# Kernel optimization log

Hardware: AMD Instinct MI355X
Metric: run time of the kernel (lower is better)

The kernel has to match this reference:

```python
import jax, jax.numpy as jnp
import numpy as np
import math

B, T, D = 2, 512, 1024
H, HD = 16, 64
F = 4096
L = 2
R = 32
LOOP_DIM = 64
TEMB = 256
MAXIT = 8
TOPK = 0.55
EPS = 1e-6


def _ste(x, q):
    # straight-through estimator: forward = q, backward = identity
    return x + jax.lax.stop_gradient(q - x)


def bitlinear(x, w, topk_ratio=None):
    # BitNet b1.58 fake-quant: ternary weights (per-tensor absmean scale),
    # int8 per-token absmax activations; optional topk activation sparsity.
    s = jnp.mean(jnp.abs(w)) + 1e-8
    wq = _ste(w, jnp.clip(jnp.round(w / s), -1.0, 1.0) * s)
    if topk_ratio is not None:
        k = max(1, int(math.ceil(topk_ratio * x.shape[-1])))
        ax = jnp.abs(x)
        thr = jax.lax.top_k(ax, k)[0][..., -1:]
        x = jnp.where(ax >= thr, x, 0.0)
    a = jnp.maximum(jnp.max(jnp.abs(x), axis=-1, keepdims=True), 1e-8)
    xq = _ste(x, jnp.clip(jnp.round(x * (127.0 / a)), -128.0, 127.0) * (a / 127.0))
    return xq @ wq.T


def rmsnorm(x, w):
    return x * jax.lax.rsqrt(jnp.mean(x * x, axis=-1, keepdims=True) + EPS) * w


def _rope(x):
    # x: (B,H,T,HD)
    half = HD // 2
    inv = 1.0 / (10000.0 ** (jnp.arange(half, dtype=jnp.float32) / half))
    ang = jnp.arange(x.shape[2], dtype=jnp.float32)[:, None] * inv[None, :]
    cos, sin = jnp.cos(ang), jnp.sin(ang)
    x1, x2 = x[..., :half], x[..., half:]
    return jnp.concatenate([x1 * cos - x2 * sin, x1 * sin + x2 * cos], axis=-1)


def bitblock(h, n1, wq, wk, wv, wo, n2, wg, wu, wd):
    # pre-norm attention + SwiGLU FFN, all projections BitLinear
    b, t, _ = h.shape
    a_in = rmsnorm(h, n1)
    heads = lambda p: p.reshape(b, t, H, HD).transpose(0, 2, 1, 3)
    q = _rope(heads(bitlinear(a_in, wq)))
    k = _rope(heads(bitlinear(a_in, wk)))
    v = heads(bitlinear(a_in, wv))
    scores = jnp.einsum('bhqd,bhkd->bhqk', q, k) / math.sqrt(HD)
    mask = jnp.tril(jnp.ones((t, t), dtype=bool))
    attn = jax.nn.softmax(jnp.where(mask, scores, -1e9), axis=-1)
    o = jnp.einsum('bhqk,bhkd->bhqd', attn, v).transpose(0, 2, 1, 3).reshape(b, t, D)
    h = h + bitlinear(o, wo)
    f_in = rmsnorm(h, n2)
    h = h + bitlinear(jax.nn.silu(bitlinear(f_in, wg)) * bitlinear(f_in, wu), wd)
    return h


def loop_delta(i, t_emb, lp_w, lp2_w, lp2_b):
    # loop_index_inject: sinusoidal loop signal gated by t_emb, padded to D
    half = LOOP_DIM // 2
    frac = i / max(MAXIT - 1, 1)
    freqs = jnp.exp(-math.log(10000.0) * jnp.arange(half, dtype=jnp.float32) / half)
    ang = frac * freqs
    sig = jnp.concatenate([jnp.sin(ang), jnp.cos(ang)])  # (LOOP_DIM,)
    comb = sig[None, :] * (t_emb @ lp_w.T) + (t_emb @ lp2_w.T + lp2_b)  # (B,LOOP_DIM)
    return jnp.pad(comb, ((0, 0), (0, D - LOOP_DIM)))[:, None, :]  # (B,1,D)


def setup_inputs() -> dict:
    key = jax.random.key(0)
    ks = jax.random.split(key, 24)
    g = lambda k, shape, sc=0.02: sc * jax.random.normal(k, shape, dtype=jnp.float32)
    return {
        'x': jax.random.normal(ks[0], (B, T, D), dtype=jnp.float32),
        'e': jax.random.normal(ks[1], (B, T, D), dtype=jnp.float32),
        't_emb': jax.random.normal(ks[2], (B, TEMB), dtype=jnp.float32),
        'blk_norm1': jnp.ones((L, D), jnp.float32),
        'blk_wq': g(ks[3], (L, D, D)),
        'blk_wk': g(ks[4], (L, D, D)),
        'blk_wv': g(ks[5], (L, D, D)),
        'blk_wo': g(ks[6], (L, D, D)),
        'blk_norm2': jnp.ones((L, D), jnp.float32),
        'blk_wg': g(ks[7], (L, F, D)),
        'blk_wu': g(ks[8], (L, F, D)),
        'blk_wd': g(ks[9], (L, D, F)),
        'A_raw': 0.1 * jax.random.normal(ks[10], (D,), dtype=jnp.float32),
        'B_w': g(ks[11], (D, D)),
        'lora_down': g(ks[12], (R, D)),
        'lora_up': g(ks[13], (D, R)),
        'iter_gate': jnp.full((MAXIT,), 0.1, jnp.float32),
        'act_w': g(ks[14], (1, D)),
        'alpha': jnp.full((MAXIT,), 1.0 / L, jnp.float32),
        'loop_proj_w': g(ks[15], (LOOP_DIM, TEMB)),
        'loop_proj2_w': g(ks[16], (LOOP_DIM, TEMB)),
        'loop_proj2_b': jnp.zeros((LOOP_DIM,), jnp.float32),
        'loop_norm_w': jnp.ones((D,), jnp.float32),
        'n_loops': 8,
    }


def reference(x, e, t_emb, blk_norm1, blk_wq, blk_wk, blk_wv, blk_wo,
              blk_norm2, blk_wg, blk_wu, blk_wd, A_raw, B_w,
              lora_down, lora_up, iter_gate, act_w, alpha,
              loop_proj_w, loop_proj2_w, loop_proj2_b, loop_norm_w, n_loops):
    A_eff = 0.99 * jnp.tanh(A_raw)          # diagonal LTI, |A|<0.99
    Be = bitlinear(e, B_w)                  # loop-invariant anchor B(e)
    h = x
    h_out = x
    ws = []
    for i in range(int(n_loops)):
        h_in = rmsnorm(h + loop_delta(i, t_emb, loop_proj_w, loop_proj2_w, loop_proj2_b), loop_norm_w)
        bo = h_in
        for l in range(L):
            bo = bitblock(bo, blk_norm1[l], blk_wq[l], blk_wk[l], blk_wv[l], blk_wo[l],
                          blk_norm2[l], blk_wg[l], blk_wu[l], blk_wd[l])
        bo = alpha[i] * bo
        h = A_eff * h + Be + bo             # LTI injection
        h = h + iter_gate[i] * bitlinear(bitlinear(h, lora_down), lora_up, topk_ratio=TOPK)
        w = jax.nn.sigmoid(bitlinear(h, act_w))  # (B,T,1) soft ACT weight
        h_out = h_out + w * (h - h_out)     # incremental residual blend
        ws.append(w)
    ponder = jnp.mean(jnp.stack(ws))
    return h_out, ponder
```

## Files before the change

### kernel.cpp

```cpp
#include <hip/hip_runtime.h>
#include <stdint.h>

#define DEV static __device__ __forceinline__

typedef float f32x4 __attribute__((ext_vector_type(4)));
typedef int   i32x4 __attribute__((ext_vector_type(4)));
typedef unsigned short u16x8 __attribute__((ext_vector_type(8)));

DEV float bf2f(unsigned short u){ return __uint_as_float(((unsigned int)u)<<16); }
DEV unsigned short f2bfr(float f){
  unsigned int u = __float_as_uint(f);
  return (unsigned short)((u + 0x7FFF + ((u>>16)&1)) >> 16);
}
DEV signed char f2i8(float f){ return (signed char)(int)f; }

DEV float wredsum(float v){
#pragma unroll
  for (int o=32;o;o>>=1) v += __shfl_xor(v,o);
  return v;
}
DEV float wredmax(float v){
#pragma unroll
  for (int o=32;o;o>>=1) v = fmaxf(v,__shfl_xor(v,o));
  return v;
}
DEV float bredsum(float v, float* red){
  v = wredsum(v);
  if ((threadIdx.x&63)==0) red[threadIdx.x>>6] = v;
  __syncthreads();
  float r = red[0]+red[1]+red[2]+red[3];
  __syncthreads();
  return r;
}
DEV float bredmax(float v, float* red){
  v = wredmax(v);
  if ((threadIdx.x&63)==0) red[threadIdx.x>>6] = v;
  __syncthreads();
  float r = fmaxf(fmaxf(red[0],red[1]),fmaxf(red[2],red[3]));
  __syncthreads();
  return r;
}

__global__ void fill_k(float* p, int n, float v){
  int i = blockIdx.x*256 + threadIdx.x;
  if (i < n) p[i] = v;
}

__global__ __launch_bounds__(256) void setup_misc_k(const float* __restrict__ x,
                                                    float* __restrict__ h, float* __restrict__ ho,
                                                    const float* __restrict__ temb,
                                                    const float* __restrict__ lpw,
                                                    const float* __restrict__ lp2w,
                                                    const float* __restrict__ lp2b,
                                                    float* __restrict__ delta,
                                                    float* __restrict__ tab){
  __shared__ float red[4];
  int bid = blockIdx.x, t = threadIdx.x;
  if (bid < 1024){
    int i = bid*256 + t;
    float4 v = *(const float4*)(x + (size_t)i*4);
    *(float4*)(h  + (size_t)i*4) = v;
    *(float4*)(ho + (size_t)i*4) = v;
    if (i==0) ho[1048576] = 0.f;
  } else if (bid < 1152){
    int blk = bid - 1024;
    int b = blk >> 6, j = blk & 63;
    float te = temb[b*256 + t];
    float p1 = bredsum(te * lpw[j*256 + t], red);
    float p2 = bredsum(te * lp2w[j*256 + t], red);
    if (t < 8){
      int i = t;
      float frac = (float)i / 7.f;
      int jj = j & 31;
      float fr = expf(-logf(10000.f) * (float)jj * (1.f/32.f));
      float ang = frac * fr;
      float sig = (j < 32) ? sinf(ang) : cosf(ang);
      delta[i*128 + b*64 + j] = sig*p1 + p2 + lp2b[j];
    }
  } else {
    int i = (bid-1152)*256 + t;
    int tpos = i >> 5, d = i & 31;
    float inv = powf(10000.f, -(float)d * (1.f/32.f));
    float sv, cv; sincosf((float)tpos * inv, &sv, &cv);
    tab[i*2]   = cv;
    tab[i*2+1] = sv;
  }
}

struct WSetup {
  const float* src[18];
  signed char* dst[18];
  int mode[18];
};
DEV long n4of(int mat){ return mat<9 ? 262144 : (mat<15 ? 1048576 : (mat<17 ? 8192 : 256)); }

__global__ __launch_bounds__(256) void absmean_all_k(WSetup wsu, float* __restrict__ part){
  __shared__ float red[4];
  int mat = blockIdx.x >> 8;
  int seg = blockIdx.x & 255;
  long n4 = n4of(mat);
  long cnt = n4 >> 8;
  const float4* p = (const float4*)wsu.src[mat] + (long)seg*cnt;
  float s0=0.f, s1=0.f, s2=0.f, s3=0.f;
  long j = threadIdx.x;
  for (; j + 768 < cnt; j += 1024){
    float4 a = p[j], b = p[j+256], c = p[j+512], d = p[j+768];
    s0 += fabsf(a.x)+fabsf(a.y)+fabsf(a.z)+fabsf(a.w);
    s1 += fabsf(b.x)+fabsf(b.y)+fabsf(b.z)+fabsf(b.w);
    s2 += fabsf(c.x)+fabsf(c.y)+fabsf(c.z)+fabsf(c.w);
    s3 += fabsf(d.x)+fabsf(d.y)+fabsf(d.z)+fabsf(d.w);
  }
  for (; j < cnt; j += 256){
    float4 a = p[j];
    s0 += fabsf(a.x)+fabsf(a.y)+fabsf(a.z)+fabsf(a.w);
  }
  float s = bredsum(s0+s1+s2+s3, red);
  if (threadIdx.x==0) part[(long)mat*256 + seg] = s;
}

__global__ __launch_bounds__(256) void finalize_scales_k(const float* __restrict__ part,
                                                         float* __restrict__ scales){
  __shared__ float red[4];
  const long numel[18] = {1048576, 1048576,1048576, 1048576,1048576, 1048576,1048576,
                          1048576,1048576, 4194304,4194304, 4194304,4194304, 4194304,4194304,
                          32768, 32768, 1024};
  for (int m=0;m<18;m++){
    float v = part[(long)m*256 + threadIdx.x];
    v = bredsum(v, red);
    if (threadIdx.x==0) scales[m] = v/(float)numel[m] + 1e-8f;
  }
  if (threadIdx.x==0){
    for (int l=0;l<2;l++){
      scales[18+l*3+0] = scales[1+l];
      scales[18+l*3+1] = scales[3+l];
      scales[18+l*3+2] = scales[5+l];
      scales[24+l*2+0] = scales[9+l];
      scales[24+l*2+1] = scales[11+l];
    }
  }
}

__global__ __launch_bounds__(256) void quantw_all_k(WSetup wsu, const float* __restrict__ scales){
  int bid = blockIdx.x;
  int mat = 0, c = 0;
  for (;;){
    int nb = mat<9 ? 256 : (mat<15 ? 1024 : (mat<17 ? 8 : 1));
    if (bid < c + nb) break;
    c += nb; mat++;
  }
  long seg = bid - c;
  long n4 = n4of(mat);
  float s = scales[mat];
  int md = wsu.mode[mat];
  const float4* src = (const float4*)wsu.src[mat];
  char4* dst = (char4*)wsu.dst[mat];
  long base = seg*1024;
#pragma unroll
  for (int k=0;k<4;k++){
    long i = base + k*256 + threadIdx.x;
    if (i < n4){
      float4 v = src[i];
      char4 q;
      q.x = f2i8(fminf(fmaxf(rintf(v.x/s), -1.f), 1.f));
      q.y = f2i8(fminf(fmaxf(rintf(v.y/s), -1.f), 1.f));
      q.z = f2i8(fminf(fmaxf(rintf(v.z/s), -1.f), 1.f));
      q.w = f2i8(fminf(fmaxf(rintf(v.w/s), -1.f), 1.f));
      if (md == 0) dst[i] = q;
      else {
        long r = i >> 8, cc = i & 255;
        dst[(((r<<1) | (md-1))<<8) | cc] = q;
      }
    }
  }
}

__global__ __launch_bounds__(256) void rowquant1k_k(const float* __restrict__ x,
                                                    signed char* __restrict__ xq,
                                                    float* __restrict__ rs){
  __shared__ float red[4];
  int m = blockIdx.x, t = threadIdx.x;
  float v[4];
  float4 f = *(const float4*)(x + (size_t)m*1024 + t*4);
  v[0]=f.x; v[1]=f.y; v[2]=f.z; v[3]=f.w;
  float am = fmaxf(fmaxf(fabsf(v[0]),fabsf(v[1])),fmaxf(fabsf(v[2]),fabsf(v[3])));
  am = bredmax(am, red);
  float a = fmaxf(am, 1e-8f), inv = 127.f/a;
  char4 q;
  q.x = f2i8(fminf(fmaxf(rintf(v[0]*inv),-128.f),127.f));
  q.y = f2i8(fminf(fmaxf(rintf(v[1]*inv),-128.f),127.f));
  q.z = f2i8(fminf(fmaxf(rintf(v[2]*inv),-128.f),127.f));
  q.w = f2i8(fminf(fmaxf(rintf(v[3]*inv),-128.f),127.f));
  *(char4*)(xq + (size_t)m*1024 + t*4) = q;
  if (t==0) rs[m] = a/127.f;
}

__global__ __launch_bounds__(256) void rowquant4k_k(const float* __restrict__ x,
                                                    signed char* __restrict__ xq,
                                                    float* __restrict__ rs){
  __shared__ float red[4];
  int m = blockIdx.x, t = threadIdx.x;
  const float* p = x + (size_t)m*4096 + t*16;
  float v[16];
#pragma unroll
  for (int j=0;j<16;j+=4){
    float4 f = *(const float4*)(p + j);
    v[j]=f.x; v[j+1]=f.y; v[j+2]=f.z; v[j+3]=f.w;
  }
  float am = 0.f;
#pragma unroll
  for (int j=0;j<16;j++) am = fmaxf(am, fabsf(v[j]));
  am = bredmax(am, red);
  float a = fmaxf(am, 1e-8f), inv = 127.f/a;
#pragma unroll
  for (int j=0;j<16;j+=4){
    char4 q;
    q.x = f2i8(fminf(fmaxf(rintf(v[j+0]*inv),-128.f),127.f));
    q.y = f2i8(fminf(fmaxf(rintf(v[j+1]*inv),-128.f),127.f));
    q.z = f2i8(fminf(fmaxf(rintf(v[j+2]*inv),-128.f),127.f));
    q.w = f2i8(fminf(fmaxf(rintf(v[j+3]*inv),-128.f),127.f));
    *(char4*)(xq + (size_t)m*4096 + t*16 + j) = q;
  }
  if (t==0) rs[m] = a/127.f;
}

__global__ __launch_bounds__(256) void loopnorm_quant_k(const float* __restrict__ h,
                                                        const float* __restrict__ delta,
                                                        const float* __restrict__ lnw,
                                                        const float* __restrict__ n1,
                                                        float* __restrict__ hin,
                                                        signed char* __restrict__ xq,
                                                        float* __restrict__ rs){
  __shared__ float red[4];
  int m = blockIdx.x, t = threadIdx.x;
  int b = m >> 9;
  float v[4];
  float4 f = *(const float4*)(h + (size_t)m*1024 + t*4);
  v[0]=f.x; v[1]=f.y; v[2]=f.z; v[3]=f.w;
  if (t < 16){
#pragma unroll
    for (int j=0;j<4;j++) v[j] += delta[b*64 + t*4 + j];
  }
  float ss = v[0]*v[0]+v[1]*v[1]+v[2]*v[2]+v[3]*v[3];
  ss = bredsum(ss, red);
  float r1 = rsqrtf(ss*(1.f/1024.f) + 1e-6f);
  float w4[4];
#pragma unroll
  for (int j=0;j<4;j++) w4[j] = v[j]*r1*lnw[t*4+j];
  float4 of; of.x=w4[0]; of.y=w4[1]; of.z=w4[2]; of.w=w4[3];
  *(float4*)(hin + (size_t)m*1024 + t*4) = of;
  float s2 = w4[0]*w4[0]+w4[1]*w4[1]+w4[2]*w4[2]+w4[3]*w4[3];
  s2 = bredsum(s2, red);
  float r2 = rsqrtf(s2*(1.f/1024.f) + 1e-6f);
  float y[4];
#pragma unroll
  for (int j=0;j<4;j++) y[j] = w4[j]*r2*n1[t*4+j];
  float am = fmaxf(fmaxf(fabsf(y[0]),fabsf(y[1])),fmaxf(fabsf(y[2]),fabsf(y[3])));
  am = bredmax(am, red);
  float a = fmaxf(am, 1e-8f), inv = 127.f/a;
  char4 q;
  q.x = f2i8(fminf(fmaxf(rintf(y[0]*inv),-128.f),127.f));
  q.y = f2i8(fminf(fmaxf(rintf(y[1]*inv),-128.f),127.f));
  q.z = f2i8(fminf(fmaxf(rintf(y[2]*inv),-128.f),127.f));
  q.w = f2i8(fminf(fmaxf(rintf(y[3]*inv),-128.f),127.f));
  *(char4*)(xq + (size_t)m*1024 + t*4) = q;
  if (t==0) rs[m] = a/127.f;
}

DEV f32x4 accfence(f32x4 c){ asm volatile("s_nop 7\n\ts_nop 7" : "+v"(c)); return c; }
DEV i32x4 accfencei(i32x4 c){ asm volatile("s_nop 7\n\ts_nop 7" : "+v"(c)); return c; }

template<bool SPLITK, bool GUSILU>
__global__ __launch_bounds__(256)
void gemm_i8(const signed char* __restrict__ A, const signed char* __restrict__ W,
             const float* __restrict__ rowsc, const float* __restrict__ wscv,
             const float* __restrict__ res, float* __restrict__ C, int N, int Kf, int Kc)
{
  __shared__ __align__(16) signed char As[2][8192];
  __shared__ __align__(16) signed char Bs[2][8192];
  const int tid = threadIdx.x;
  const int lane = tid & 63, wvid = tid >> 6;
  const int wr = wvid >> 1, wc = wvid & 1;
  const int bm = blockIdx.y, bn = blockIdx.x;

  const int r0 = (wvid<<4) + (lane>>2);
  const int sw = (((lane&3) ^ ((r0>>1)&3)) << 4);
  const long kstart = SPLITK ? (long)blockIdx.z * Kc : 0;
  const signed char* gA = A + (size_t)(bm*128 + r0)*Kf + kstart + sw;
  const signed char* gB = W + (size_t)(bn*128 + r0)*Kf + kstart + sw;
  const size_t row64 = (size_t)64*Kf;

#define STAGE(buf, koff) do { \
    __builtin_amdgcn_global_load_lds(gA + (koff),         &As[buf][(wvid<<10)],      16, 0, 0); \
    __builtin_amdgcn_global_load_lds(gA + (koff) + row64, &As[buf][(wvid<<10)+4096], 16, 0, 0); \
    __builtin_amdgcn_global_load_lds(gB + (koff),         &Bs[buf][(wvid<<10)],      16, 0, 0); \
    __builtin_amdgcn_global_load_lds(gB + (koff) + row64, &Bs[buf][(wvid<<10)+4096], 16, 0, 0); \
  } while(0)

  i32x4 acc[4][4] = {};
  const int rA = (wr<<6) + (lane&15);
  const int rB = (wc<<6) + (lane&15);
  const int psA = (((lane>>4) ^ (((lane&15)>>1)&3)) << 4);

  STAGE(0, 0);
  const int NT = Kc >> 6;
  int cur = 0;
  for (int kt = 0; kt < NT; ++kt){
    const int knext = (kt+1 < NT) ? ((kt+1)<<6) : 0;
    STAGE(cur^1, knext);
    asm volatile("s_waitcnt vmcnt(4)" ::: "memory");
    __builtin_amdgcn_s_barrier();
    asm volatile("" ::: "memory");
    i32x4 a[4], b[4];
    const signed char* Ab = As[cur];
    const signed char* Bb = Bs[cur];
#pragma unroll
    for (int mi=0;mi<4;mi++) a[mi] = *(const i32x4*)(Ab + (rA + mi*16)*64 + psA);
#pragma unroll
    for (int ni=0;ni<4;ni++) b[ni] = *(const i32x4*)(Bb + (rB + ni*16)*64 + psA);
#pragma unroll
    for (int mi=0;mi<4;mi++)
#pragma unroll
      for (int ni=0;ni<4;ni++)
        asm("v_mfma_i32_16x16x64_i8 %0, %1, %2, %0" : "+v"(acc[mi][ni]) : "v"(a[mi]), "v"(b[ni]));
    asm volatile("s_waitcnt lgkmcnt(0)" ::: "memory");
    __builtin_amdgcn_s_barrier();
    cur ^= 1;
  }
#undef STAGE

#pragma unroll
  for (int mi=0;mi<4;mi++)
#pragma unroll
    for (int ni=0;ni<4;ni++)
      acc[mi][ni] = accfencei(acc[mi][ni]);

  const int rif = (lane>>4)<<2;
  const int cif = lane&15;
  const int gcol0 = bn*128 + (wc<<6);

  if constexpr (SPLITK){
    float* P = C + (size_t)blockIdx.z * ((size_t)N << 10);
#pragma unroll
    for (int mi=0;mi<4;mi++)
#pragma unroll
      for (int r=0;r<4;r++){
        const int grow = bm*128 + (wr<<6) + mi*16 + rif + r;
#pragma unroll
        for (int ni=0;ni<4;ni++)
          P[(size_t)grow*N + gcol0 + ni*16 + cif] = (float)acc[mi][ni][r];
      }
    return;
  }

  if constexpr (GUSILU){
    const float sg = wscv[0], su = wscv[1];
#pragma unroll
    for (int mi=0;mi<4;mi++){
#pragma unroll
      for (int r=0;r<4;r++){
        const int grow = bm*128 + (wr<<6) + mi*16 + rif + r;
        const float rsc = rowsc[grow];
#pragma unroll
        for (int ni=0;ni<4;ni++){
          const int gcol = gcol0 + ni*16 + cif;
          float val = (float)acc[mi][ni][r] * rsc * ((gcol & 1) ? su : sg);
          float other = __shfl_xor(val, 1);
          if (!(lane & 1)){
            float g = val, u = other;
            float outv = g/(1.f+expf(-g))*u;
            C[(size_t)grow*4096 + (gcol>>1)] = outv;
          }
        }
      }
    }
    return;
  }

#pragma unroll
  for (int mi=0;mi<4;mi++){
#pragma unroll
    for (int r=0;r<4;r++){
      const int grow = bm*128 + (wr<<6) + mi*16 + rif + r;
      const float rsc = rowsc[grow];
#pragma unroll
      for (int ni=0;ni<4;ni++){
        const int gcol = gcol0 + ni*16 + cif;
        float vvv = (float)acc[mi][ni][r] * rsc * wscv[0];
        const size_t off = (size_t)grow*N + gcol;
        if (res) vvv += res[off];
        C[off] = vvv;
      }
    }
  }
}

__global__ __launch_bounds__(256) void reduce4_k(const float* __restrict__ P,
                                                 const float* __restrict__ rowsc,
                                                 const float* __restrict__ wsc,
                                                 const float* __restrict__ res,
                                                 float* __restrict__ C){
  int m = blockIdx.x, t = threadIdx.x;
  float s0 = rowsc[m] * wsc[0];
  size_t off = (size_t)m*1024 + t*4;
  float4 a = *(const float4*)(P + off);
  float4 b = *(const float4*)(P + 1048576 + off);
  float4 c = *(const float4*)(P + 2097152 + off);
  float4 d = *(const float4*)(P + 3145728 + off);
  float4 o;
  o.x = (a.x+b.x+c.x+d.x)*s0;
  o.y = (a.y+b.y+c.y+d.y)*s0;
  o.z = (a.z+b.z+c.z+d.z)*s0;
  o.w = (a.w+b.w+c.w+d.w)*s0;
  if (res){
    float4 r = *(const float4*)(res + off);
    o.x += r.x; o.y += r.y; o.z += r.z; o.w += r.w;
  }
  *(float4*)(C + off) = o;
}

__global__ __launch_bounds__(256) void redq_norm_k(const float* __restrict__ P,
                                                   const float* rowsc,
                                                   const float* __restrict__ wsc,
                                                   const float* __restrict__ res,
                                                   const float* __restrict__ gamma,
                                                   float* __restrict__ Cout,
                                                   signed char* __restrict__ xq,
                                                   float* rs){
  __shared__ float red[4];
  int m = blockIdx.x, t = threadIdx.x;
  float s0 = rowsc[m] * wsc[0];
  size_t off = (size_t)m*1024 + t*4;
  float4 a = *(const float4*)(P + off);
  float4 b = *(const float4*)(P + 1048576 + off);
  float4 c = *(const float4*)(P + 2097152 + off);
  float4 d = *(const float4*)(P + 3145728 + off);
  float4 r4 = *(const float4*)(res + off);
  float v[4];
  v[0] = r4.x + (a.x+b.x+c.x+d.x)*s0;
  v[1] = r4.y + (a.y+b.y+c.y+d.y)*s0;
  v[2] = r4.z + (a.z+b.z+c.z+d.z)*s0;
  v[3] = r4.w + (a.w+b.w+c.w+d.w)*s0;
  float4 of; of.x=v[0]; of.y=v[1]; of.z=v[2]; of.w=v[3];
  *(float4*)(Cout + off) = of;
  float ss = v[0]*v[0]+v[1]*v[1]+v[2]*v[2]+v[3]*v[3];
  ss = bredsum(ss, red);
  float r1 = rsqrtf(ss*(1.f/1024.f) + 1e-6f);
  float y[4];
#pragma unroll
  for (int j=0;j<4;j++) y[j] = v[j]*r1*gamma[t*4+j];
  float am = fmaxf(fmaxf(fabsf(y[0]),fabsf(y[1])),fmaxf(fabsf(y[2]),fabsf(y[3])));
  am = bredmax(am, red);
  float aq = fmaxf(am, 1e-8f), inv = 127.f/aq;
  char4 q;
  q.x = f2i8(fminf(fmaxf(rintf(y[0]*inv),-128.f),127.f));
  q.y = f2i8(fminf(fmaxf(rintf(y[1]*inv),-128.f),127.f));
  q.z = f2i8(fminf(fmaxf(rintf(y[2]*inv),-128.f),127.f));
  q.w = f2i8(fminf(fmaxf(rintf(y[3]*inv),-128.f),127.f));
  *(char4*)(xq + (size_t)m*1024 + t*4) = q;
  if (t==0) rs[m] = aq/127.f;
}

__global__ __launch_bounds__(256) void redfin_k(const float* __restrict__ P,
                                                const float* __restrict__ rowsc,
                                                const float* __restrict__ wsc,
                                                const float* __restrict__ res,
                                                float* __restrict__ h,
                                                const float* __restrict__ Be,
                                                const float* __restrict__ Araw,
                                                const float* __restrict__ alpha, int it,
                                                const signed char* __restrict__ ldq,
                                                const float* __restrict__ sld,
                                                const signed char* __restrict__ luq,
                                                const float* __restrict__ slu,
                                                const signed char* __restrict__ actq,
                                                const float* __restrict__ sact,
                                                const float* __restrict__ ig,
                                                float* __restrict__ hout,
                                                float* __restrict__ ponder,
                                                const float* __restrict__ dnext,
                                                const float* __restrict__ lnw,
                                                const float* __restrict__ n1,
                                                float* __restrict__ hin,
                                                signed char* __restrict__ xqn,
                                                float* __restrict__ rsn,
                                                int doNext){
  __shared__ float red[4];
  __shared__ float xrow[1024];
  __shared__ float part[256];
  __shared__ float xs[32];
  __shared__ float sh_thr, sh_gs;
  int m = blockIdx.x, t = threadIdx.x;
  float al = alpha[it];
  float s0 = rowsc[m] * wsc[0];
  size_t off = (size_t)m*1024 + t*4;
  float4 a = *(const float4*)(P + off);
  float4 b = *(const float4*)(P + 1048576 + off);
  float4 c = *(const float4*)(P + 2097152 + off);
  float4 d = *(const float4*)(P + 3145728 + off);
  float4 r4 = *(const float4*)(res + off);
  float4 hh = *(const float4*)(h + off);
  float4 be = *(const float4*)(Be + off);
  float4 ar = *(const float4*)(Araw + t*4);
  float v[4];
  v[0] = 0.99f*tanhf(ar.x)*hh.x + be.x + al*(r4.x + (a.x+b.x+c.x+d.x)*s0);
  v[1] = 0.99f*tanhf(ar.y)*hh.y + be.y + al*(r4.y + (a.y+b.y+c.y+d.y)*s0);
  v[2] = 0.99f*tanhf(ar.z)*hh.z + be.z + al*(r4.z + (a.z+b.z+c.z+d.z)*s0);
  v[3] = 0.99f*tanhf(ar.w)*hh.w + be.w + al*(r4.w + (a.w+b.w+c.w+d.w)*s0);
  float am = fmaxf(fmaxf(fabsf(v[0]),fabsf(v[1])),fmaxf(fabsf(v[2]),fabsf(v[3])));
  am = bredmax(am, red);
  float aq = fmaxf(am, 1e-8f), inv = 127.f/aq;
#pragma unroll
  for (int j=0;j<4;j++) xrow[t*4+j] = fminf(fmaxf(rintf(v[j]*inv),-128.f),127.f);
  float rsv = aq/127.f;
  __syncthreads();
  {
    int r = t & 31, seg = t >> 5;
    const signed char* wrow = ldq + (size_t)r*1024 + seg*128;
    const float* xr = xrow + seg*128;
    float acc = 0.f;
    for (int k=0;k<128;k+=4){
      char4 w4 = *(const char4*)(wrow + k);
      acc += xr[k]*(float)w4.x + xr[k+1]*(float)w4.y + xr[k+2]*(float)w4.z + xr[k+3]*(float)w4.w;
    }
    part[t] = acc;
  }
  __syncthreads();
  if (t < 32){
    float s = 0.f;
    for (int sg=0; sg<8; sg++) s += part[sg*32 + t];
    xs[t] = s * rsv * (*sld);
  }
  __syncthreads();
  float val = 0.f, av = 0.f, amax = 0.f;
  if (t < 32){
    val = xs[t]; av = fabsf(val);
    int rank = 0;
    for (int j=0;j<32;j++){
      float aj = fabsf(xs[j]);
      amax = fmaxf(amax, aj);
      if (aj > av || (aj == av && j < t)) rank++;
    }
    if (rank == 17) sh_thr = av;
  }
  __syncthreads();
  if (t < 32){
    float a2 = fmaxf(amax, 1e-8f);
    float q = 0.f;
    if (av >= sh_thr) q = fminf(fmaxf(rintf(val*(127.f/a2)), -128.f), 127.f);
    xs[t] = q;
    if (t == 0) sh_gs = ig[it] * (*slu) * (a2/127.f);
  }
  __syncthreads();
  float gs = sh_gs;
  float hn[4];
  int n0 = t*4;
#pragma unroll
  for (int ni=0;ni<4;ni++){
    const signed char* lr = luq + (size_t)(n0+ni)*32;
    float dd = 0.f;
    for (int k=0;k<32;k+=4){
      char4 w4 = *(const char4*)(lr + k);
      dd += xs[k]*(float)w4.x + xs[k+1]*(float)w4.y + xs[k+2]*(float)w4.z + xs[k+3]*(float)w4.w;
    }
    hn[ni] = v[ni] + gs*dd;
  }
  float am2 = fmaxf(fmaxf(fabsf(hn[0]),fabsf(hn[1])),fmaxf(fabsf(hn[2]),fabsf(hn[3])));
  am2 = bredmax(am2, red);
  float a2 = fmaxf(am2, 1e-8f), inv2 = 127.f/a2;
  float zp = 0.f;
#pragma unroll
  for (int ni=0;ni<4;ni++){
    float q = fminf(fmaxf(rintf(hn[ni]*inv2),-128.f),127.f);
    zp += q * (float)actq[n0+ni];
  }
  zp = bredsum(zp, red);
  float z = zp * (a2/127.f) * (*sact);
  float wv = 1.f/(1.f+expf(-z));
#pragma unroll
  for (int ni=0;ni<4;ni++){
    size_t o2 = (size_t)m*1024 + n0+ni;
    float ho = hout[o2];
    hout[o2] = ho + wv*(hn[ni]-ho);
    h[o2] = hn[ni];
  }
  if (t==0) atomicAdd(ponder, wv * (1.f/8192.f));

  if (doNext){
    int b2 = m >> 9;
    float v2[4] = {hn[0], hn[1], hn[2], hn[3]};
    if (t < 16){
#pragma unroll
      for (int j=0;j<4;j++) v2[j] += dnext[b2*64 + t*4 + j];
    }
    float ss2 = v2[0]*v2[0]+v2[1]*v2[1]+v2[2]*v2[2]+v2[3]*v2[3];
    ss2 = bredsum(ss2, red);
    float r1 = rsqrtf(ss2*(1.f/1024.f) + 1e-6f);
    float w4[4];
#pragma unroll
    for (int j=0;j<4;j++) w4[j] = v2[j]*r1*lnw[t*4+j];
    float4 of; of.x=w4[0]; of.y=w4[1]; of.z=w4[2]; of.w=w4[3];
    *(float4*)(hin + off) = of;
    float s2 = w4[0]*w4[0]+w4[1]*w4[1]+w4[2]*w4[2]+w4[3]*w4[3];
    s2 = bredsum(s2, red);
    float r2 = rsqrtf(s2*(1.f/1024.f) + 1e-6f);
    float y[4];
#pragma unroll
    for (int j=0;j<4;j++) y[j] = w4[j]*r2*n1[t*4+j];
    float am3 = fmaxf(fmaxf(fabsf(y[0]),fabsf(y[1])),fmaxf(fabsf(y[2]),fabsf(y[3])));
    am3 = bredmax(am3, red);
    float aq3 = fmaxf(am3, 1e-8f), inv3 = 127.f/aq3;
    char4 q;
    q.x = f2i8(fminf(fmaxf(rintf(y[0]*inv3),-128.f),127.f));
    q.y = f2i8(fminf(fmaxf(rintf(y[1]*inv3),-128.f),127.f));
    q.z = f2i8(fminf(fmaxf(rintf(y[2]*inv3),-128.f),127.f));
    q.w = f2i8(fminf(fmaxf(rintf(y[3]*inv3),-128.f),127.f));
    *(char4*)(xqn + off) = q;
    if (t==0) rsn[m] = aq3/127.f;
  }
}

__global__ __launch_bounds__(256) void rope_reduce_k(const float* P,
                                                     const float* __restrict__ rs,
                                                     const float* __restrict__ wscv,
                                                     const float* __restrict__ tab,
                                                     unsigned short* __restrict__ C){
  int m = blockIdx.x, t = threadIdx.x;
  const float rsc = rs[m];
  const int tpos = m & 511;
  const size_t base = (size_t)m*3072;
  const float* P1 = P + 3145728;
  int p0 = t*4;
  int hh = p0 >> 5, d = p0 & 31;
  int c1 = hh*64 + d;
  float wsc = wscv[c1>>10] * rsc * ((c1 < 1024) ? 0.125f : 1.f);
  float4 xa0 = *(const float4*)(P  + base + c1);
  float4 xa1 = *(const float4*)(P1 + base + c1);
  float4 xb0 = *(const float4*)(P  + base + c1 + 32);
  float4 xb1 = *(const float4*)(P1 + base + c1 + 32);
  float4 cs01 = *(const float4*)(tab + ((size_t)tpos*32 + d)*2);
  float4 cs23 = *(const float4*)(tab + ((size_t)tpos*32 + d)*2 + 4);
  int cv = 2048 + t*4;
  float4 va = *(const float4*)(P  + base + cv);
  float4 vb = *(const float4*)(P1 + base + cv);
  float wv2 = wscv[2] * rsc;

  float x1[4] = {(xa0.x+xa1.x)*wsc, (xa0.y+xa1.y)*wsc, (xa0.z+xa1.z)*wsc, (xa0.w+xa1.w)*wsc};
  float x2[4] = {(xb0.x+xb1.x)*wsc, (xb0.y+xb1.y)*wsc, (xb0.z+xb1.z)*wsc, (xb0.w+xb1.w)*wsc};
  float cc[4] = {cs01.x, cs01.z, cs23.x, cs23.z};
  float ss[4] = {cs01.y, cs01.w, cs23.y, cs23.w};
  ushort4 o1, o2, ov;
  o1.x = f2bfr(x1[0]*cc[0] - x2[0]*ss[0]);  o2.x = f2bfr(x1[0]*ss[0] + x2[0]*cc[0]);
  o1.y = f2bfr(x1[1]*cc[1] - x2[1]*ss[1]);  o2.y = f2bfr(x1[1]*ss[1] + x2[1]*cc[1]);
  o1.z = f2bfr(x1[2]*cc[2] - x2[2]*ss[2]);  o2.z = f2bfr(x1[2]*ss[2] + x2[2]*cc[2]);
  o1.w = f2bfr(x1[3]*cc[3] - x2[3]*ss[3]);  o2.w = f2bfr(x1[3]*ss[3] + x2[3]*cc[3]);
  ov.x = f2bfr((va.x+vb.x)*wv2); ov.y = f2bfr((va.y+vb.y)*wv2);
  ov.z = f2bfr((va.z+vb.z)*wv2); ov.w = f2bfr((va.w+vb.w)*wv2);
  *(ushort4*)(C + base + c1)      = o1;
  *(ushort4*)(C + base + c1 + 32) = o2;
  *(ushort4*)(C + base + cv)      = ov;
}

DEV int swz64(int r, int c){ return r*64 + (c ^ ((r&7)<<3)); }

__global__ __launch_bounds__(256) void attn_bf16_k(const unsigned short* __restrict__ qkv,
                                                   float* __restrict__ o){
  __shared__ __align__(16) unsigned short Qs[4096];
  __shared__ __align__(16) unsigned short Ks[4096];
  __shared__ __align__(16) unsigned short Vt[4096];
  __shared__ __align__(16) unsigned short Ps[4][1024];
  const int tid = threadIdx.x;
  const int lane = tid & 63, wv = tid >> 6;
  const int qt = blockIdx.x & 7, bh = blockIdx.x >> 3;
  const int b = bh >> 4, h = bh & 15;
  const int tokb = b*512;
  const int l15 = lane & 15, lh = lane >> 4;

  {
    int r = tid >> 2, c0 = (tid & 3) << 4;
    const unsigned short* s = qkv + (size_t)(tokb + qt*64 + r)*3072 + h*64 + c0;
    u16x8 f0 = *(const u16x8*)s, f1 = *(const u16x8*)(s+8);
    *(u16x8*)(Qs + swz64(r, c0))   = f0;
    *(u16x8*)(Qs + swz64(r, c0+8)) = f1;
  }

  float m_run[4] = {-1e30f,-1e30f,-1e30f,-1e30f};
  float l_run[4] = {0.f,0.f,0.f,0.f};
  f32x4 accO[4] = {};

  for (int kt = 0; kt <= qt; ++kt){
    __syncthreads();
    {
      int r = tid >> 2, c0 = (tid & 3) << 4;
      const unsigned short* s = qkv + (size_t)(tokb + kt*64 + r)*3072 + 1024 + h*64 + c0;
      u16x8 f0 = *(const u16x8*)s, f1 = *(const u16x8*)(s+8);
      *(u16x8*)(Ks + swz64(r, c0))   = f0;
      *(u16x8*)(Ks + swz64(r, c0+8)) = f1;
    }
    {
      int r0 = (tid >> 3) << 1, cv = (tid & 7) << 3;
      const unsigned short* s0 = qkv + (size_t)(tokb + kt*64 + r0)*3072 + 2048 + h*64 + cv;
      u16x8 a = *(const u16x8*)s0;
      u16x8 b2 = *(const u16x8*)(s0 + 3072);
#pragma unroll
      for (int j=0;j<8;j++){
        int d = cv + j;
        unsigned int pk = (unsigned int)a[j] | ((unsigned int)b2[j]<<16);
        *(unsigned int*)(Vt + swz64(d, r0)) = pk;
      }
    }
    __syncthreads();

    f32x4 s4[4] = {};
#pragma unroll
    for (int kc=0; kc<2; ++kc){
      i32x4 aq = *(const i32x4*)(Qs + swz64(wv*16 + l15, kc*32 + lh*8));
#pragma unroll
      for (int nt=0; nt<4; ++nt){
        i32x4 bk = *(const i32x4*)(Ks + swz64(nt*16 + l15, kc*32 + lh*8));
        asm("v_mfma_f32_16x16x32_bf16 %0, %1, %2, %0" : "+v"(s4[nt]) : "v"(aq), "v"(bk));
      }
    }
#pragma unroll
    for (int nt=0; nt<4; ++nt) s4[nt] = accfence(s4[nt]);

    const bool diag = (kt == qt);
    float sf[4];
#pragma unroll
    for (int r=0;r<4;r++){
      int rl = lh*4 + r;
      float mx = -1e30f;
#pragma unroll
      for (int nt=0; nt<4; ++nt){
        float v = s4[nt][r];
        if (diag && (nt*16 + l15) > (wv*16 + rl)) v = -1e30f;
        s4[nt][r] = v;
        mx = fmaxf(mx, v);
      }
      mx = fmaxf(mx, __shfl_xor(mx,1));
      mx = fmaxf(mx, __shfl_xor(mx,2));
      mx = fmaxf(mx, __shfl_xor(mx,4));
      mx = fmaxf(mx, __shfl_xor(mx,8));
      float mn = fmaxf(m_run[r], mx);
      sf[r] = __expf(m_run[r] - mn);
      m_run[r] = mn;
      float ps = 0.f;
#pragma unroll
      for (int nt=0; nt<4; ++nt){
        float p = __expf(s4[nt][r] - mn);
        ps += p;
        Ps[wv][swz64(rl, nt*16 + l15)] = f2bfr(p);
      }
      ps += __shfl_xor(ps,1); ps += __shfl_xor(ps,2);
      ps += __shfl_xor(ps,4); ps += __shfl_xor(ps,8);
      l_run[r] = l_run[r]*sf[r] + ps;
    }
#pragma unroll
    for (int dt=0; dt<4; ++dt){
#pragma unroll
      for (int r=0;r<4;r++) accO[dt][r] *= sf[r];
      accO[dt] = accfence(accO[dt]);
    }
#pragma unroll
    for (int kc=0; kc<2; ++kc){
      i32x4 pa = *(const i32x4*)(Ps[wv] + swz64(l15, kc*32 + lh*8));
#pragma unroll
      for (int dt=0; dt<4; ++dt){
        i32x4 vb3 = *(const i32x4*)(Vt + swz64(dt*16 + l15, kc*32 + lh*8));
        asm("v_mfma_f32_16x16x32_bf16 %0, %1, %2, %0" : "+v"(accO[dt]) : "v"(pa), "v"(vb3));
      }
    }
  }
#pragma unroll
  for (int dt=0; dt<4; ++dt) accO[dt] = accfence(accO[dt]);
#pragma unroll
  for (int r=0;r<4;r++){
    float invl = 1.f / l_run[r];
    int row = qt*64 + wv*16 + lh*4 + r;
    float* op = o + (size_t)(tokb + row)*1024 + h*64 + l15;
#pragma unroll
    for (int dt=0; dt<4; ++dt)
      op[dt*16] = accO[dt][r] * invl;
  }
}

extern "C" void kernel_launch(void* const* d_in, const int* in_sizes, int n_in,
                              void* d_out, int out_size, void* d_ws, size_t ws_size,
                              hipStream_t stream)
{
  (void)in_sizes; (void)n_in;
  const float* x     = (const float*)d_in[0];
  const float* e     = (const float*)d_in[1];
  const float* temb  = (const float*)d_in[2];
  const float* bn1   = (const float*)d_in[3];
  const float* bwq   = (const float*)d_in[4];
  const float* bwk   = (const float*)d_in[5];
  const float* bwv   = (const float*)d_in[6];
  const float* bwo   = (const float*)d_in[7];
  const float* bn2   = (const float*)d_in[8];
  const float* bwg   = (const float*)d_in[9];
  const float* bwu   = (const float*)d_in[10];
  const float* bwd   = (const float*)d_in[11];
  const float* Araw  = (const float*)d_in[12];
  const float* Bw    = (const float*)d_in[13];
  const float* ldw   = (const float*)d_in[14];
  const float* luw   = (const float*)d_in[15];
  const float* ig    = (const float*)d_in[16];
  const float* actw  = (const float*)d_in[17];
  const float* alph  = (const float*)d_in[18];
  const float* lpw   = (const float*)d_in[19];
  const float* lp2w  = (const float*)d_in[20];
  const float* lp2b  = (const float*)d_in[21];
  const float* lnw   = (const float*)d_in[22];

  char* ws = (char*)d_ws;
  float* out = (float*)d_out;
  const size_t WS_NEEDED = 94600704ull;
  if (ws_size < WS_NEEDED){
    fill_k<<<(out_size+255)/256,256,0,stream>>>(out, out_size, 1.0e9f);
    return;
  }

  signed char* qw_qkv = (signed char*)(ws + 0);
  signed char* qw_wo  = (signed char*)(ws + 6291456);
  signed char* qw_gu  = (signed char*)(ws + 8388608);
  signed char* qw_wd  = (signed char*)(ws + 25165824);
  signed char* qw_bw  = (signed char*)(ws + 33554432);
  signed char* qw_ld  = (signed char*)(ws + 34603008);
  signed char* qw_lu  = (signed char*)(ws + 34635776);
  signed char* qw_act = (signed char*)(ws + 34668544);
  float* scales = (float*)(ws + 34669568);
  float* part   = (float*)(ws + 34670080);
  float* delta  = (float*)(ws + 34688512);
  float* hbuf   = (float*)(ws + 34692608);
  float* Bebuf  = (float*)(ws + 38886912);
  float* bufX   = (float*)(ws + 43081216);
  float* bufY   = (float*)(ws + 47275520);
  float* gub    = (float*)(ws + 51469824);
  unsigned short* qkv_bf = (unsigned short*)(ws + 76635648);
  float* obuf   = (float*)(ws + 85024256);
  signed char* xq1k = (signed char*)(ws + 89218560);
  float* rs1k   = (float*)(ws + 90267136);
  signed char* xqm  = (signed char*)(ws + 90271232);
  float* rsm    = (float*)(ws + 94465536);
  float* ropetab= (float*)(ws + 94469632);

  WSetup wsu;
  wsu.src[0]=Bw;
  wsu.src[1]=bwq; wsu.src[2]=bwq+1048576;
  wsu.src[3]=bwk; wsu.src[4]=bwk+1048576;
  wsu.src[5]=bwv; wsu.src[6]=bwv+1048576;
  wsu.src[7]=bwo; wsu.src[8]=bwo+1048576;
  wsu.src[9]=bwg; wsu.src[10]=bwg+4194304;
  wsu.src[11]=bwu; wsu.src[12]=bwu+4194304;
  wsu.src[13]=bwd; wsu.src[14]=bwd+4194304;
  wsu.src[15]=ldw; wsu.src[16]=luw; wsu.src[17]=actw;
  wsu.dst[0]=qw_bw;
  wsu.dst[1]=qw_qkv;             wsu.dst[2]=qw_qkv+3145728;
  wsu.dst[3]=qw_qkv+1048576;     wsu.dst[4]=qw_qkv+3145728+1048576;
  wsu.dst[5]=qw_qkv+2097152;     wsu.dst[6]=qw_qkv+3145728+2097152;
  wsu.dst[7]=qw_wo;              wsu.dst[8]=qw_wo+1048576;
  wsu.dst[9]=qw_gu;              wsu.dst[10]=qw_gu+8388608;
  wsu.dst[11]=qw_gu;             wsu.dst[12]=qw_gu+8388608;
  wsu.dst[13]=qw_wd;             wsu.dst[14]=qw_wd+4194304;
  wsu.dst[15]=qw_ld; wsu.dst[16]=qw_lu; wsu.dst[17]=qw_act;
  for (int i=0;i<18;i++) wsu.mode[i]=0;
  wsu.mode[9]=1;  wsu.mode[10]=1;
  wsu.mode[11]=2; wsu.mode[12]=2;

  absmean_all_k<<<4608,256,0,stream>>>(wsu, part);
  finalize_scales_k<<<1,256,0,stream>>>(part, scales);
  quantw_all_k<<<8465,256,0,stream>>>(wsu, scales);

  setup_misc_k<<<1216,256,0,stream>>>(x, hbuf, out, temb, lpw, lp2w, lp2b, delta, ropetab);

  rowquant1k_k<<<1024,256,0,stream>>>(e, xq1k, rs1k);
  { dim3 g(8,8,4); gemm_i8<true,false><<<g,256,0,stream>>>(xq1k, qw_bw, nullptr, nullptr, nullptr, gub, 1024, 1024, 256); }
  reduce4_k<<<1024,256,0,stream>>>(gub, rs1k, scales+0, nullptr, Bebuf);

  for (int it=0; it<8; ++it){
    if (it==0)
      loopnorm_quant_k<<<1024,256,0,stream>>>(hbuf, delta, lnw, bn1, bufX, xq1k, rs1k);
    for (int l=0;l<2;l++){
      { dim3 g(24,8,2); gemm_i8<true,false><<<g,256,0,stream>>>(xq1k, qw_qkv + (size_t)l*3145728, nullptr, nullptr, nullptr, gub, 3072, 1024, 512); }
      rope_reduce_k<<<1024,256,0,stream>>>(gub, rs1k, scales+18+l*3, ropetab, qkv_bf);
      attn_bf16_k<<<256,256,0,stream>>>(qkv_bf, obuf);
      rowquant1k_k<<<1024,256,0,stream>>>(obuf, xq1k, rs1k);
      { dim3 g(8,8,4); gemm_i8<true,false><<<g,256,0,stream>>>(xq1k, qw_wo + (size_t)l*1048576, nullptr, nullptr, nullptr, gub, 1024, 1024, 256); }
      redq_norm_k<<<1024,256,0,stream>>>(gub, rs1k, scales+7+l, bufX, bn2 + (size_t)l*1024, bufY, xq1k, rs1k);
      { dim3 g(64,8); gemm_i8<false,true><<<g,256,0,stream>>>(xq1k, qw_gu + (size_t)l*8388608, rs1k, scales+24+l*2, nullptr, gub, 8192, 1024, 1024); }
      rowquant4k_k<<<1024,256,0,stream>>>(gub, xqm, rsm);
      { dim3 g(8,8,4); gemm_i8<true,false><<<g,256,0,stream>>>(xqm, qw_wd + (size_t)l*4194304, nullptr, nullptr, nullptr, gub, 1024, 4096, 1024); }
      if (l==0){
        redq_norm_k<<<1024,256,0,stream>>>(gub, rsm, scales+13, bufY, bn1 + 1024, bufX, xq1k, rs1k);
      } else {
        redfin_k<<<1024,256,0,stream>>>(gub, rsm, scales+14, bufY, hbuf, Bebuf, Araw, alph, it,
                                        qw_ld, scales+15, qw_lu, scales+16, qw_act, scales+17,
                                        ig, out, out + 1048576,
                                        delta + (it+1 < 8 ? (it+1)*128 : 0), lnw, bn1, bufX, xq1k, rs1k,
                                        (it < 7) ? 1 : 0);
      }
    }
  }
}
```

Measured before the change: 2.121 ms.

## Fuse RoPE and scaling into a dedicated QKV int8 GEMM without split-K

Replaces the split-K QKV GEMM and the separate rope_reduce kernel with one GEMM that runs the full K=1024 per block. Its epilogue applies the row and weight scales and RoPE, then writes bf16 directly. This removes the fp32 partial-sum buffer round-trip and one launch per layer, at the cost of halving the grid (192 blocks) and using a longer K loop per block. It also unrolls the weight absmean reduction to issue twice as many loads per iteration on large matrices.

```diff
diff --git a/kernel.cpp b/kernel.cpp
--- a/kernel.cpp
+++ b/kernel.cpp
@@ -102,17 +102,35 @@
   long cnt = n4 >> 8;
   const float4* p = (const float4*)wsu.src[mat] + (long)seg*cnt;
   float s0=0.f, s1=0.f, s2=0.f, s3=0.f;
-  long j = threadIdx.x;
-  for (; j + 768 < cnt; j += 1024){
-    float4 a = p[j], b = p[j+256], c = p[j+512], d = p[j+768];
-    s0 += fabsf(a.x)+fabsf(a.y)+fabsf(a.z)+fabsf(a.w);
-    s1 += fabsf(b.x)+fabsf(b.y)+fabsf(b.z)+fabsf(b.w);
-    s2 += fabsf(c.x)+fabsf(c.y)+fabsf(c.z)+fabsf(c.w);
-    s3 += fabsf(d.x)+fabsf(d.y)+fabsf(d.z)+fabsf(d.w);
-  }
-  for (; j < cnt; j += 256){
-    float4 a = p[j];
-    s0 += fabsf(a.x)+fabsf(a.y)+fabsf(a.z)+fabsf(a.w);
+  if (cnt >= 2048){
+    long half = cnt >> 1;
+    const float4* q = p + half;
+    long j = threadIdx.x;
+    for (; j + 768 < half; j += 1024){
+      float4 a = p[j], b = p[j+256], c = p[j+512], d = p[j+768];
+      float4 e = q[j], f = q[j+256], g = q[j+512], h2 = q[j+768];
+      s0 += fabsf(a.x)+fabsf(a.y)+fabsf(a.z)+fabsf(a.w) + fabsf(e.x)+fabsf(e.y)+fabsf(e.z)+fabsf(e.w);
+      s1 += fabsf(b.x)+fabsf(b.y)+fabsf(b.z)+fabsf(b.w) + fabsf(f.x)+fabsf(f.y)+fabsf(f.z)+fabsf(f.w);
+      s2 += fabsf(c.x)+fabsf(c.y)+fabsf(c.z)+fabsf(c.w) + fabsf(g.x)+fabsf(g.y)+fabsf(g.z)+fabsf(g.w);
+      s3 += fabsf(d.x)+fabsf(d.y)+fabsf(d.z)+fabsf(d.w) + fabsf(h2.x)+fabsf(h2.y)+fabsf(h2.z)+fabsf(h2.w);
+    }
+    for (; j < half; j += 256){
+      float4 a = p[j], e = q[j];
+      s0 += fabsf(a.x)+fabsf(a.y)+fabsf(a.z)+fabsf(a.w) + fabsf(e.x)+fabsf(e.y)+fabsf(e.z)+fabsf(e.w);
+    }
+  } else {
+    long j = threadIdx.x;
+    for (; j + 768 < cnt; j += 1024){
+      float4 a = p[j], b = p[j+256], c = p[j+512], d = p[j+768];
+      s0 += fabsf(a.x)+fabsf(a.y)+fabsf(a.z)+fabsf(a.w);
+      s1 += fabsf(b.x)+fabsf(b.y)+fabsf(b.z)+fabsf(b.w);
+      s2 += fabsf(c.x)+fabsf(c.y)+fabsf(c.z)+fabsf(c.w);
+      s3 += fabsf(d.x)+fabsf(d.y)+fabsf(d.z)+fabsf(d.w);
+    }
+    for (; j < cnt; j += 256){
+      float4 a = p[j];
+      s0 += fabsf(a.x)+fabsf(a.y)+fabsf(a.z)+fabsf(a.w);
+    }
   }
   float s = bredsum(s0+s1+s2+s3, red);
   if (threadIdx.x==0) part[(long)mat*256 + seg] = s;
@@ -389,6 +407,110 @@
         const size_t off = (size_t)grow*N + gcol;
         if (res) vvv += res[off];
         C[off] = vvv;
+      }
+    }
+  }
+}
+
+__global__ __launch_bounds__(256)
+void gemm_qkv128(const signed char* __restrict__ A, const signed char* __restrict__ W,
+                 const float* __restrict__ rowsc, const float* __restrict__ wscv,
+                 const float* __restrict__ tab, unsigned short* __restrict__ C)
+{
+  __shared__ __align__(16) signed char As[2][8192];
+  __shared__ __align__(16) signed char Bs[2][8192];
+  const int tid = threadIdx.x;
+  const int lane = tid & 63, wvid = tid >> 6;
+  const int wr = wvid >> 1, wc = wvid & 1;
+  const int bm = blockIdx.y, bn = blockIdx.x;
+  const int Kf = 1024;
+
+  const int r0 = (wvid<<4) + (lane>>2);
+  const int sw = (((lane&3) ^ ((r0>>1)&3)) << 4);
+  const signed char* gA = A + (size_t)(bm*128 + r0)*Kf + sw;
+  const signed char* gB = W + (size_t)(bn*128 + r0)*Kf + sw;
+  const size_t row64 = (size_t)64*Kf;
+
+#define STAGE(buf, koff) do { \
+    __builtin_amdgcn_global_load_lds(gA + (koff),         &As[buf][(wvid<<10)],      16, 0, 0); \
+    __builtin_amdgcn_global_load_lds(gA + (koff) + row64, &As[buf][(wvid<<10)+4096], 16, 0, 0); \
+    __builtin_amdgcn_global_load_lds(gB + (koff),         &Bs[buf][(wvid<<10)],      16, 0, 0); \
+    __builtin_amdgcn_global_load_lds(gB + (koff) + row64, &Bs[buf][(wvid<<10)+4096], 16, 0, 0); \
+  } while(0)
+
+  i32x4 acc[4][4] = {};
+  const int rA = (wr<<6) + (lane&15);
+  const int rB = (wc<<6) + (lane&15);
+  const int psA = (((lane>>4) ^ (((lane&15)>>1)&3)) << 4);
+
+  STAGE(0, 0);
+  const int NT = 16;
+  int cur = 0;
+  for (int kt = 0; kt < NT; ++kt){
+    const int knext = (kt+1 < NT) ? ((kt+1)<<6) : 0;
+    STAGE(cur^1, knext);
+    asm volatile("s_waitcnt vmcnt(4)" ::: "memory");
+    __builtin_amdgcn_s_barrier();
+    asm volatile("" ::: "memory");
+    i32x4 a[4], b[4];
+    const signed char* Ab = As[cur];
+    const signed char* Bb = Bs[cur];
+#pragma unroll
+    for (int mi=0;mi<4;mi++) a[mi] = *(const i32x4*)(Ab + (rA + mi*16)*64 + psA);
+#pragma unroll
+    for (int ni=0;ni<4;ni++) b[ni] = *(const i32x4*)(Bb + (rB + ni*16)*64 + psA);
+#pragma unroll
+    for (int mi=0;mi<4;mi++)
+#pragma unroll
+      for (int ni=0;ni<4;ni++)
+        asm("v_mfma_i32_16x16x64_i8 %0, %1, %2, %0" : "+v"(acc[mi][ni]) : "v"(a[mi]), "v"(b[ni]));
+    asm volatile("s_waitcnt lgkmcnt(0)" ::: "memory");
+    __builtin_amdgcn_s_barrier();
+    cur ^= 1;
+  }
+#undef STAGE
+
+#pragma unroll
+  for (int mi=0;mi<4;mi++)
+#pragma unroll
+    for (int ni=0;ni<4;ni++)
+      acc[mi][ni] = accfencei(acc[mi][ni]);
+
+  const int rif = (lane>>4)<<2;
+  const int cif = lane&15;
+  const int gcol0 = bn*128 + (wc<<6);
+  const int sec = gcol0 >> 10;
+  const float wsc = wscv[sec] * ((sec==0) ? 0.125f : 1.f);
+
+  if (sec < 2){
+#pragma unroll
+    for (int mi=0;mi<4;mi++){
+#pragma unroll
+      for (int r=0;r<4;r++){
+        const int grow = bm*128 + (wr<<6) + mi*16 + rif + r;
+        const float s = rowsc[grow] * wsc;
+        const int tpos = grow & 511;
+#pragma unroll
+        for (int np=0;np<2;np++){
+          const int d = np*16 + cif;
+          float2 cs = *(const float2*)(tab + (size_t)((tpos<<5) + d)*2);
+          float x1 = (float)acc[mi][np][r]   * s;
+          float x2 = (float)acc[mi][np+2][r] * s;
+          C[(size_t)grow*3072 + gcol0 + d]      = f2bfr(x1*cs.x - x2*cs.y);
+          C[(size_t)grow*3072 + gcol0 + 32 + d] = f2bfr(x1*cs.y + x2*cs.x);
+        }
+      }
+    }
+  } else {
+#pragma unroll
+    for (int mi=0;mi<4;mi++){
+#pragma unroll
+      for (int r=0;r<4;r++){
+        const int grow = bm*128 + (wr<<6) + mi*16 + rif + r;
+        const float s = rowsc[grow] * wsc;
+#pragma unroll
+        for (int ni=0;ni<4;ni++)
+          C[(size_t)grow*3072 + gcol0 + ni*16 + cif] = f2bfr((float)acc[mi][ni][r] * s);
       }
     }
   }
@@ -619,47 +741,6 @@
   }
 }
 
-__global__ __launch_bounds__(256) void rope_reduce_k(const float* P,
-                                                     const float* __restrict__ rs,
-                                                     const float* __restrict__ wscv,
-                                                     const float* __restrict__ tab,
-                                                     unsigned short* __restrict__ C){
-  int m = blockIdx.x, t = threadIdx.x;
-  const float rsc = rs[m];
-  const int tpos = m & 511;
-  const size_t base = (size_t)m*3072;
-  const float* P1 = P + 3145728;
-  int p0 = t*4;
-  int hh = p0 >> 5, d = p0 & 31;
-  int c1 = hh*64 + d;
-  float wsc = wscv[c1>>10] * rsc * ((c1 < 1024) ? 0.125f : 1.f);
-  float4 xa0 = *(const float4*)(P  + base + c1);
-  float4 xa1 = *(const float4*)(P1 + base + c1);
-  float4 xb0 = *(const float4*)(P  + base + c1 + 32);
-  float4 xb1 = *(const float4*)(P1 + base + c1 + 32);
-  float4 cs01 = *(const float4*)(tab + ((size_t)tpos*32 + d)*2);
-  float4 cs23 = *(const float4*)(tab + ((size_t)tpos*32 + d)*2 + 4);
-  int cv = 2048 + t*4;
-  float4 va = *(const float4*)(P  + base + cv);
-  float4 vb = *(const float4*)(P1 + base + cv);
-  float wv2 = wscv[2] * rsc;
-
-  float x1[4] = {(xa0.x+xa1.x)*wsc, (xa0.y+xa1.y)*wsc, (xa0.z+xa1.z)*wsc, (xa0.w+xa1.w)*wsc};
-  float x2[4] = {(xb0.x+xb1.x)*wsc, (xb0.y+xb1.y)*wsc, (xb0.z+xb1.z)*wsc, (xb0.w+xb1.w)*wsc};
-  float cc[4] = {cs01.x, cs01.z, cs23.x, cs23.z};
-  float ss[4] = {cs01.y, cs01.w, cs23.y, cs23.w};
-  ushort4 o1, o2, ov;
-  o1.x = f2bfr(x1[0]*cc[0] - x2[0]*ss[0]);  o2.x = f2bfr(x1[0]*ss[0] + x2[0]*cc[0]);
-  o1.y = f2bfr(x1[1]*cc[1] - x2[1]*ss[1]);  o2.y = f2bfr(x1[1]*ss[1] + x2[1]*cc[1]);
-  o1.z = f2bfr(x1[2]*cc[2] - x2[2]*ss[2]);  o2.z = f2bfr(x1[2]*ss[2] + x2[2]*cc[2]);
-  o1.w = f2bfr(x1[3]*cc[3] - x2[3]*ss[3]);  o2.w = f2bfr(x1[3]*ss[3] + x2[3]*cc[3]);
-  ov.x = f2bfr((va.x+vb.x)*wv2); ov.y = f2bfr((va.y+vb.y)*wv2);
-  ov.z = f2bfr((va.z+vb.z)*wv2); ov.w = f2bfr((va.w+vb.w)*wv2);
-  *(ushort4*)(C + base + c1)      = o1;
-  *(ushort4*)(C + base + c1 + 32) = o2;
-  *(ushort4*)(C + base + cv)      = ov;
-}
-
 DEV int swz64(int r, int c){ return r*64 + (c ^ ((r&7)<<3)); }
 
 __global__ __launch_bounds__(256) void attn_bf16_k(const unsigned short* __restrict__ qkv,
@@ -881,8 +962,7 @@
     if (it==0)
       loopnorm_quant_k<<<1024,256,0,stream>>>(hbuf, delta, lnw, bn1, bufX, xq1k, rs1k);
     for (int l=0;l<2;l++){
-      { dim3 g(24,8,2); gemm_i8<true,false><<<g,256,0,stream>>>(xq1k, qw_qkv + (size_t)l*3145728, nullptr, nullptr, nullptr, gub, 3072, 1024, 512); }
-      rope_reduce_k<<<1024,256,0,stream>>>(gub, rs1k, scales+18+l*3, ropetab, qkv_bf);
+      { dim3 g(24,8); gemm_qkv128<<<g,256,0,stream>>>(xq1k, qw_qkv + (size_t)l*3145728, rs1k, scales+18+l*3, ropetab, qkv_bf); }
       attn_bf16_k<<<256,256,0,stream>>>(qkv_bf, obuf);
       rowquant1k_k<<<1024,256,0,stream>>>(obuf, xq1k, rs1k);
       { dim3 g(8,8,4); gemm_i8<true,false><<<g,256,0,stream>>>(xq1k, qw_wo + (size_t)l*1048576, nullptr, nullptr, nullptr, gub, 1024, 1024, 256); }
```

Result: faster. 2.024 ms (-4.6%).
